# Kernel tuning notes

Measured on AMD Instinct MI355X. Metric: run time of the kernel, lower is better.

## Reference

```python
import jax, jax.numpy as jnp
import numpy as np

N, C, T, V = 64, 64, 300, 25  # batch, channels, frames, joints
CO = 64
EPS = 1e-5


def setup_inputs() -> dict:
    key = jax.random.key(0)
    ks = jax.random.split(key, 5)
    x = jax.random.normal(ks[0], (N, C, T, V), dtype=jnp.float32)
    lin_w = jax.random.normal(ks[1], (C, CO), dtype=jnp.float32) * np.sqrt(1.0 / CO)
    lin_b = jnp.zeros((1, 1, CO), dtype=jnp.float32)
    feat_mask = jax.random.normal(ks[2], (1, V, C), dtype=jnp.float32) * 0.1
    bn_gamma = jnp.ones((V * CO,), dtype=jnp.float32)
    bn_beta = jnp.zeros((V * CO,), dtype=jnp.float32)
    shift_in = jax.random.randint(ks[3], (V * C,), 0, V * C, dtype=jnp.int32)
    shift_out = jax.random.randint(ks[4], (V * CO,), 0, V * CO, dtype=jnp.int32)
    return {"x": x, "lin_w": lin_w, "lin_b": lin_b, "feat_mask": feat_mask,
            "bn_gamma": bn_gamma, "bn_beta": bn_beta,
            "shift_in": shift_in, "shift_out": shift_out}


def reference(x, lin_w, lin_b, feat_mask, bn_gamma, bn_beta, shift_in, shift_out):
    n, c, t, v = x.shape
    co = lin_w.shape[1]
    # (N,C,T,V) -> (N*T, V*C)
    xt = jnp.transpose(x, (0, 2, 3, 1)).reshape(n * t, v * c)
    # shift-in gather along feature axis
    xs = jnp.take(xt, shift_in, axis=1).reshape(n * t, v, c)
    # learned feature mask (tanh + 1)
    xs = xs * (jnp.tanh(feat_mask) + 1.0)
    # small channel-mixing matmul + bias
    y = jnp.einsum('nvc,cd->nvd', xs, lin_w) + lin_b  # (N*T, V, CO)
    y = y.reshape(n * t, v * co)
    # shift-out gather
    y = jnp.take(y, shift_out, axis=1)
    # BatchNorm1d (training mode: batch statistics over N*T)
    mean = jnp.mean(y, axis=0)
    var = jnp.mean(jnp.square(y - mean), axis=0)
    y = (y - mean) * jax.lax.rsqrt(var + EPS) * bn_gamma + bn_beta
    # back to (N, CO, T, V), residual (in==out -> identity down), ReLU
    y = jnp.transpose(y.reshape(n, t, v, co), (0, 3, 1, 2))
    return jax.nn.relu(y + x)
```

## Files before the change

### kernel.cpp

```cpp
#include <hip/hip_runtime.h>

typedef __bf16 bf16x8 __attribute__((ext_vector_type(8)));
typedef float f32x4 __attribute__((ext_vector_type(4)));
typedef unsigned short u16;
typedef unsigned int u32;
typedef unsigned long long u64;
typedef u16 u16x8 __attribute__((ext_vector_type(8)));

#define TID ((int)threadIdx.x)

constexpr int Nn = 64, Tt = 300, Vv = 25;
constexpr int Fin = 1600;
constexpr int RowsT = 19200;
constexpr int TBR = 16;
constexpr int NTB = 19;
constexpr int NBLK = Nn * NTB;
constexpr int RAWE = 64 * TBR * Vv;
constexpr float EPSv = 1e-5f;

constexpr int WS_EPI   = 12800;
constexpr int WS_WV    = 25600;
constexpr int WS_COMBO = 33792;
constexpr int WS_PART  = 40192;
constexpr size_t WS_NEED_PART = (size_t)WS_PART + (size_t)NBLK * 3200 * 4;

__device__ __forceinline__ u16 f2b(float f) {
  u32 u = __float_as_uint(f);
  return (u16)((u + 0x7fffu + ((u >> 16) & 1u)) >> 16);
}
__device__ __forceinline__ float b2f(u16 h) {
  return __uint_as_float(((u32)h) << 16);
}
__device__ __forceinline__ u64 pack4(float a, float b, float c, float d) {
  return (u64)f2b(a) | ((u64)f2b(b) << 16) | ((u64)f2b(c) << 32) | ((u64)f2b(d) << 48);
}

__device__ __forceinline__ void stage_raw(const float* __restrict__ x,
                                          int n, int t0, int validg, u16* raw) {
  const int base = n * 480000 + t0 * 25;
  if (validg == TBR * 25) {
    #pragma unroll
    for (int i = 0; i < 13; ++i) {
      int q = TID + i * 512;
      if (q < 6400) {
        int c = q / 100;
        int g4 = (q - c * 100) * 4;
        float4 xv = *reinterpret_cast<const float4*>(x + base + c * 7500 + g4);
        *reinterpret_cast<u64*>(raw + q * 4) = pack4(xv.x, xv.y, xv.z, xv.w);
      }
    }
  } else {
    #pragma unroll
    for (int i = 0; i < 13; ++i) {
      int q = TID + i * 512;
      if (q < 6400) {
        int c = q / 100;
        int g4 = (q - c * 100) * 4;
        float4 xv = make_float4(0.f, 0.f, 0.f, 0.f);
        if (g4 < validg)
          xv = *reinterpret_cast<const float4*>(x + base + c * 7500 + g4);
        *reinterpret_cast<u64*>(raw + q * 4) = pack4(xv.x, xv.y, xv.z, xv.w);
      }
    }
  }
}

__device__ __forceinline__ void load_bfr_g(const u16* __restrict__ wv, bf16x8 bfr[2][4]) {
  int l = TID & 63;
  #pragma unroll
  for (int ks = 0; ks < 2; ++ks)
    #pragma unroll
    for (int nt = 0; nt < 4; ++nt)
      bfr[ks][nt] = *reinterpret_cast<const bf16x8*>(wv + ((((ks << 2) | nt) << 9) + l * 8));
}

__device__ __forceinline__ bf16x8 build_a(const u16* raw, const u32* __restrict__ combo,
                                          int v, int ks, int t, int grp) {
  int jb = v * 64 + ks * 32 + grp * 8;
  bf16x8 a;
  #pragma unroll
  for (int i = 0; i < 8; ++i) {
    u32 cb = combo[jb + i];
    float m = __uint_as_float((cb & 0xffffu) << 16);
    float xv = b2f(raw[(cb >> 16) + t * 25]);
    a[i] = (__bf16)(xv * m);
  }
  return a;
}

__global__ void k_wv(const float* __restrict__ lin_w, const float* __restrict__ feat_mask,
                     const int* __restrict__ shift_in, float* __restrict__ wsum,
                     u16* __restrict__ wv, u32* __restrict__ combo_g) {
  int gid = blockIdx.x * 256 + TID;
  if (gid < 3200) wsum[gid] = 0.f;
  if (gid < Fin) {
    int s = shift_in[gid];
    u32 off = (u32)((s & 63) * 400 + (s >> 6));
    float m = tanhf(feat_mask[gid]) + 1.0f;
    combo_g[gid] = (off << 16) | (u32)f2b(m);
  }
  if (gid >= 2048 && gid < 2560) {
    int t = gid - 2048;
    int l = t & 63, nt = (t >> 6) & 3, ks = t >> 8;
    int c0 = ks * 32 + (l >> 4) * 8, d = nt * 16 + (l & 15);
    u16x8 o8;
    #pragma unroll
    for (int i = 0; i < 8; ++i) o8[i] = f2b(lin_w[(c0 + i) * 64 + d]);
    *reinterpret_cast<u16x8*>(wv + ((((ks << 2) | nt) << 9) + l * 8)) = o8;
  }
}

template <int ATOMIC>
__global__ __launch_bounds__(512, 6) void k_stats(
    const float* __restrict__ x, const u16* __restrict__ wv,
    const u32* __restrict__ combo_g, float* __restrict__ target)
{
  __shared__ __align__(16) u16 raw[RAWE];
  int bid = blockIdx.x;
  int n = bid / NTB, tb = bid - n * NTB;
  int t0 = tb * TBR;
  int validg = min(TBR, Tt - t0) * 25;
  int w = TID >> 6, l = TID & 63;
  int t_lane = l & 15, grp = l >> 4;

  stage_raw(x, n, t0, validg, raw);
  __syncthreads();

  bf16x8 areg[4][2];
  #pragma unroll
  for (int k = 0; k < 4; ++k) {
    int v = w + 8 * k;
    if (v < Vv) {
      areg[k][0] = build_a(raw, combo_g, v, 0, t_lane, grp);
      areg[k][1] = build_a(raw, combo_g, v, 1, t_lane, grp);
    }
  }

  bf16x8 bfr[2][4];
  load_bfr_g(wv, bfr);

  float* pb = target + (ATOMIC ? 0 : bid * 3200);
  #pragma unroll
  for (int k = 0; k < 4; ++k) {
    int v = w + 8 * k;
    if (v < Vv) {
      float pr[4], qr[4];
      #pragma unroll
      for (int nt = 0; nt < 4; ++nt) {
        f32x4 acc = {0.f, 0.f, 0.f, 0.f};
        acc = __builtin_amdgcn_mfma_f32_16x16x32_bf16(areg[k][0], bfr[0][nt], acc, 0, 0, 0);
        acc = __builtin_amdgcn_mfma_f32_16x16x32_bf16(areg[k][1], bfr[1][nt], acc, 0, 0, 0);
        float pp = acc[0] + acc[1] + acc[2] + acc[3];
        float qq = acc[0]*acc[0] + acc[1]*acc[1] + acc[2]*acc[2] + acc[3]*acc[3];
        pp += __shfl_xor(pp, 16); pp += __shfl_xor(pp, 32);
        qq += __shfl_xor(qq, 16); qq += __shfl_xor(qq, 32);
        pr[nt] = pp; qr[nt] = qq;
      }
      if (ATOMIC) {
        if ((l & 48) == 0) {
          #pragma unroll
          for (int nt = 0; nt < 4; ++nt) {
            int col = v * 64 + nt * 16 + t_lane;
            atomicAdd(&pb[col], pr[nt]);
            atomicAdd(&pb[1600 + col], qr[nt]);
          }
        }
      } else {
        float pv = (grp & 2) ? ((grp & 1) ? pr[3] : pr[2]) : ((grp & 1) ? pr[1] : pr[0]);
        float qv = (grp & 2) ? ((grp & 1) ? qr[3] : qr[2]) : ((grp & 1) ? qr[1] : qr[0]);
        pb[v * 64 + l] = pv;
        pb[1600 + v * 64 + l] = qv;
      }
    }
  }
}

__global__ __launch_bounds__(256) void k_red(const float* __restrict__ part,
                                             float* __restrict__ wsum) {
  __shared__ float red[16 * 17];
  int col0 = blockIdx.x * 16;
  int c = TID & 15, ch = TID >> 4;
  float s = 0.f;
  int r0 = ch * 76;
  #pragma unroll 4
  for (int i = 0; i < 76; ++i) s += part[(r0 + i) * 3200 + col0 + c];
  red[ch * 17 + c] = s;
  __syncthreads();
  if (TID < 16) {
    float t = 0.f;
    #pragma unroll
    for (int j = 0; j < 16; ++j) t += red[j * 17 + TID];
    wsum[col0 + TID] = t;
  }
}

__global__ void k_epi(const float* __restrict__ wsum, const float* __restrict__ gamma,
                      const float* __restrict__ beta, const int* __restrict__ shift_out,
                      u64* __restrict__ epi_g) {
  int k = blockIdx.x * 256 + TID;
  if (k >= Fin) return;
  int s2 = shift_out[k];
  float sm = wsum[s2] * (1.0f / RowsT);
  float sq = wsum[1600 + s2] * (1.0f / RowsT);
  float rstd = rsqrtf(fmaxf(sq - sm * sm, 0.f) + EPSv);
  float sc = gamma[k] * rstd;
  int d = k & 63, v = k >> 6;
  epi_g[d * 25 + v] = (u64)__float_as_uint(sc)
                    | ((u64)f2b(beta[k] - sm * sc) << 32)
                    | ((u64)(u32)(s2 * 16) << 48);
}

__global__ __launch_bounds__(512, 6) void k_main(
    const float* __restrict__ x, const u16* __restrict__ wv,
    const u32* __restrict__ combo_g, const u64* __restrict__ epi_g,
    float* __restrict__ out)
{
  __shared__ __align__(16) u16 smem[RAWE];
  u16* raw  = smem;
  u16* ylds = smem;

  int bid = blockIdx.x;
  int n = bid / NTB, tb = bid - n * NTB;
  int t0 = tb * TBR;
  int validg = min(TBR, Tt - t0) * 25;

  stage_raw(x, n, t0, validg, raw);
  __syncthreads();

  int w = TID >> 6, l = TID & 63, grp = l >> 4, t_lane = l & 15;
  bf16x8 areg[4][2];
  #pragma unroll
  for (int k = 0; k < 4; ++k) {
    int v = w + 8 * k;
    if (v < Vv) {
      areg[k][0] = build_a(raw, combo_g, v, 0, t_lane, grp);
      areg[k][1] = build_a(raw, combo_g, v, 1, t_lane, grp);
    }
  }
  __syncthreads();

  bf16x8 bfr[2][4];
  load_bfr_g(wv, bfr);

  #pragma unroll
  for (int k = 0; k < 4; ++k) {
    int v = w + 8 * k;
    if (v < Vv) {
      #pragma unroll
      for (int nt = 0; nt < 4; ++nt) {
        f32x4 acc = {0.f, 0.f, 0.f, 0.f};
        acc = __builtin_amdgcn_mfma_f32_16x16x32_bf16(areg[k][0], bfr[0][nt], acc, 0, 0, 0);
        acc = __builtin_amdgcn_mfma_f32_16x16x32_bf16(areg[k][1], bfr[1][nt], acc, 0, 0, 0);
        int col = v * 64 + nt * 16 + t_lane;
        int o = (col << 4) + ((grp ^ (col & 3)) << 2);
        *reinterpret_cast<u64*>(ylds + o) = pack4(acc[0], acc[1], acc[2], acc[3]);
      }
    }
  }
  __syncthreads();

  const int obase = n * 480000 + t0 * 25;
  #pragma unroll 2
  for (int it = 0; it < 13; ++it) {
    int g = TID + it * 512;
    if (g < 6400) {
      int d = g / 100;
      int f0 = (g - d * 100) * 4;
      if (f0 < validg) {
        const float4 xr = *reinterpret_cast<const float4*>(x + obase + d * 7500 + f0);
        float4 o;
        float* op = &o.x;
        const float* xp = &xr.x;
        #pragma unroll
        for (int e = 0; e < 4; ++e) {
          int f = f0 + e;
          int t = f / 25;
          int v = f - t * 25;
          u64 ep = epi_g[d * 25 + v];
          float sc = __uint_as_float((u32)ep);
          float of = b2f((u16)(ep >> 32));
          u32 bk = (u32)(ep >> 48);
          int elem = (int)bk + (t ^ (((bk >> 4) & 3) << 2));
          float y = b2f(ylds[elem]);
          op[e] = fmaxf(fmaf(y, sc, of) + xp[e], 0.f);
        }
        *reinterpret_cast<float4*>(out + obase + d * 7500 + f0) = o;
      }
    }
  }
}

extern "C" void kernel_launch(void* const* d_in, const int* in_sizes, int n_in,
                              void* d_out, int out_size, void* d_ws, size_t ws_size,
                              hipStream_t stream) {
  (void)in_sizes; (void)n_in; (void)out_size;
  const float* x        = (const float*)d_in[0];
  const float* lin_w    = (const float*)d_in[1];
  const float* feat_mask= (const float*)d_in[3];
  const float* gamma    = (const float*)d_in[4];
  const float* beta     = (const float*)d_in[5];
  const int*   shift_in = (const int*)d_in[6];
  const int*   shift_out= (const int*)d_in[7];
  float* wsum   = (float*)d_ws;
  u64*   epi_g  = (u64*)((char*)d_ws + WS_EPI);
  u16*   wv     = (u16*)((char*)d_ws + WS_WV);
  u32*   combo_g= (u32*)((char*)d_ws + WS_COMBO);
  float* part   = (float*)((char*)d_ws + WS_PART);

  k_wv<<<13, 256, 0, stream>>>(lin_w, feat_mask, shift_in, wsum, wv, combo_g);
  if (ws_size >= WS_NEED_PART) {
    k_stats<0><<<NBLK, 512, 0, stream>>>(x, wv, combo_g, part);
    k_red<<<200, 256, 0, stream>>>(part, wsum);
  } else {
    k_stats<1><<<NBLK, 512, 0, stream>>>(x, wv, combo_g, wsum);
  }
  k_epi <<<7, 256, 0, stream>>>(wsum, gamma, beta, shift_out, epi_g);
  k_main<<<NBLK, 512, 0, stream>>>(x, wv, combo_g, epi_g, (float*)d_out);
}
```

Measured before the change: 132.9 us.

## Retile time blocks to 12 frames, drop tail padding, stage epilogue table in LDS

Time tiles shrink from 16 frames to 12, so the 300 frames split evenly into 25 blocks. This removes the padded tail block and its bounds checks, and cuts the zero work done inside 16-row MFMA tiles. The y buffer in LDS moves to a row-major layout with padded stride 1604, and the epilogue scale/offset/index table is copied into LDS instead of being read from global memory per element. In exchange, a quarter of every MFMA tile is wasted on masked rows, and per-block LDS use and block count both rise.

```diff
diff --git a/kernel.cpp b/kernel.cpp
--- a/kernel.cpp
+++ b/kernel.cpp
@@ -12,10 +12,13 @@
 constexpr int Nn = 64, Tt = 300, Vv = 25;
 constexpr int Fin = 1600;
 constexpr int RowsT = 19200;
-constexpr int TBR = 16;
-constexpr int NTB = 19;
+constexpr int TBR = 12;
+constexpr int NTB = 25;
 constexpr int NBLK = Nn * NTB;
-constexpr int RAWE = 64 * TBR * Vv;
+constexpr int RAWE = 64 * 300;
+constexpr int YROW = 1604;
+constexpr int EPI_OFF = 38496;
+constexpr int SMEM_SZ = EPI_OFF + 12800;
 constexpr float EPSv = 1e-5f;
 
 constexpr int WS_EPI   = 12800;
@@ -36,31 +39,16 @@
 }
 
 __device__ __forceinline__ void stage_raw(const float* __restrict__ x,
-                                          int n, int t0, int validg, u16* raw) {
-  const int base = n * 480000 + t0 * 25;
-  if (validg == TBR * 25) {
-    #pragma unroll
-    for (int i = 0; i < 13; ++i) {
-      int q = TID + i * 512;
-      if (q < 6400) {
-        int c = q / 100;
-        int g4 = (q - c * 100) * 4;
-        float4 xv = *reinterpret_cast<const float4*>(x + base + c * 7500 + g4);
-        *reinterpret_cast<u64*>(raw + q * 4) = pack4(xv.x, xv.y, xv.z, xv.w);
-      }
-    }
-  } else {
-    #pragma unroll
-    for (int i = 0; i < 13; ++i) {
-      int q = TID + i * 512;
-      if (q < 6400) {
-        int c = q / 100;
-        int g4 = (q - c * 100) * 4;
-        float4 xv = make_float4(0.f, 0.f, 0.f, 0.f);
-        if (g4 < validg)
-          xv = *reinterpret_cast<const float4*>(x + base + c * 7500 + g4);
-        *reinterpret_cast<u64*>(raw + q * 4) = pack4(xv.x, xv.y, xv.z, xv.w);
-      }
+                                          int n, int tb, u16* raw) {
+  const int base = n * 480000 + tb * 300;
+  #pragma unroll
+  for (int i = 0; i < 10; ++i) {
+    int q = TID + i * 512;
+    if (q < 4800) {
+      int c = q / 75;
+      int g4 = (q - c * 75) * 4;
+      float4 xv = *reinterpret_cast<const float4*>(x + base + c * 7500 + g4);
+      *reinterpret_cast<u64*>(raw + q * 4) = pack4(xv.x, xv.y, xv.z, xv.w);
     }
   }
 }
@@ -84,6 +72,10 @@
     float m = __uint_as_float((cb & 0xffffu) << 16);
     float xv = b2f(raw[(cb >> 16) + t * 25]);
     a[i] = (__bf16)(xv * m);
+  }
+  if (t >= TBR) {
+    u64* p = reinterpret_cast<u64*>(&a);
+    p[0] = 0; p[1] = 0;
   }
   return a;
 }
@@ -95,7 +87,7 @@
   if (gid < 3200) wsum[gid] = 0.f;
   if (gid < Fin) {
     int s = shift_in[gid];
-    u32 off = (u32)((s & 63) * 400 + (s >> 6));
+    u32 off = (u32)((s & 63) * 300 + (s >> 6));
     float m = tanhf(feat_mask[gid]) + 1.0f;
     combo_g[gid] = (off << 16) | (u32)f2b(m);
   }
@@ -118,12 +110,10 @@
   __shared__ __align__(16) u16 raw[RAWE];
   int bid = blockIdx.x;
   int n = bid / NTB, tb = bid - n * NTB;
-  int t0 = tb * TBR;
-  int validg = min(TBR, Tt - t0) * 25;
   int w = TID >> 6, l = TID & 63;
   int t_lane = l & 15, grp = l >> 4;
 
-  stage_raw(x, n, t0, validg, raw);
+  stage_raw(x, n, tb, raw);
   __syncthreads();
 
   bf16x8 areg[4][2];
@@ -181,9 +171,9 @@
   int col0 = blockIdx.x * 16;
   int c = TID & 15, ch = TID >> 4;
   float s = 0.f;
-  int r0 = ch * 76;
+  int r0 = ch * 100;
   #pragma unroll 4
-  for (int i = 0; i < 76; ++i) s += part[(r0 + i) * 3200 + col0 + c];
+  for (int i = 0; i < 100; ++i) s += part[(r0 + i) * 3200 + col0 + c];
   red[ch * 17 + c] = s;
   __syncthreads();
   if (TID < 16) {
@@ -207,7 +197,7 @@
   int d = k & 63, v = k >> 6;
   epi_g[d * 25 + v] = (u64)__float_as_uint(sc)
                     | ((u64)f2b(beta[k] - sm * sc) << 32)
-                    | ((u64)(u32)(s2 * 16) << 48);
+                    | ((u64)(u32)s2 << 48);
 }
 
 __global__ __launch_bounds__(512, 6) void k_main(
@@ -215,16 +205,20 @@
     const u32* __restrict__ combo_g, const u64* __restrict__ epi_g,
     float* __restrict__ out)
 {
-  __shared__ __align__(16) u16 smem[RAWE];
-  u16* raw  = smem;
-  u16* ylds = smem;
+  __shared__ __align__(16) unsigned char smem[SMEM_SZ];
+  u16* raw  = reinterpret_cast<u16*>(smem);
+  u16* ylds = reinterpret_cast<u16*>(smem);
+  u64* epi  = reinterpret_cast<u64*>(smem + EPI_OFF);
 
   int bid = blockIdx.x;
   int n = bid / NTB, tb = bid - n * NTB;
-  int t0 = tb * TBR;
-  int validg = min(TBR, Tt - t0) * 25;
-
-  stage_raw(x, n, t0, validg, raw);
+
+  stage_raw(x, n, tb, raw);
+  #pragma unroll
+  for (int i = 0; i < 4; ++i) {
+    int j = TID + i * 512;
+    if (j < Fin) epi[j] = epi_g[j];
+  }
   __syncthreads();
 
   int w = TID >> 6, l = TID & 63, grp = l >> 4, t_lane = l & 15;
@@ -251,41 +245,40 @@
         f32x4 acc = {0.f, 0.f, 0.f, 0.f};
         acc = __builtin_amdgcn_mfma_f32_16x16x32_bf16(areg[k][0], bfr[0][nt], acc, 0, 0, 0);
         acc = __builtin_amdgcn_mfma_f32_16x16x32_bf16(areg[k][1], bfr[1][nt], acc, 0, 0, 0);
-        int col = v * 64 + nt * 16 + t_lane;
-        int o = (col << 4) + ((grp ^ (col & 3)) << 2);
-        *reinterpret_cast<u64*>(ylds + o) = pack4(acc[0], acc[1], acc[2], acc[3]);
+        if (grp < 3) {
+          int col = v * 64 + nt * 16 + t_lane;
+          #pragma unroll
+          for (int j = 0; j < 4; ++j)
+            ylds[(grp * 4 + j) * YROW + col] = f2b(acc[j]);
+        }
       }
     }
   }
   __syncthreads();
 
-  const int obase = n * 480000 + t0 * 25;
-  #pragma unroll 2
-  for (int it = 0; it < 13; ++it) {
+  const int obase = n * 480000 + tb * 300;
+  #pragma unroll
+  for (int it = 0; it < 10; ++it) {
     int g = TID + it * 512;
-    if (g < 6400) {
-      int d = g / 100;
-      int f0 = (g - d * 100) * 4;
-      if (f0 < validg) {
-        const float4 xr = *reinterpret_cast<const float4*>(x + obase + d * 7500 + f0);
-        float4 o;
-        float* op = &o.x;
-        const float* xp = &xr.x;
-        #pragma unroll
-        for (int e = 0; e < 4; ++e) {
-          int f = f0 + e;
-          int t = f / 25;
-          int v = f - t * 25;
-          u64 ep = epi_g[d * 25 + v];
-          float sc = __uint_as_float((u32)ep);
-          float of = b2f((u16)(ep >> 32));
-          u32 bk = (u32)(ep >> 48);
-          int elem = (int)bk + (t ^ (((bk >> 4) & 3) << 2));
-          float y = b2f(ylds[elem]);
-          op[e] = fmaxf(fmaf(y, sc, of) + xp[e], 0.f);
-        }
-        *reinterpret_cast<float4*>(out + obase + d * 7500 + f0) = o;
+    if (g < 4800) {
+      int d = g / 75;
+      int f0 = (g - d * 75) * 4;
+      const float4 xr = *reinterpret_cast<const float4*>(x + obase + d * 7500 + f0);
+      float4 o;
+      float* op = &o.x;
+      const float* xp = &xr.x;
+      #pragma unroll
+      for (int e = 0; e < 4; ++e) {
+        int f = f0 + e;
+        int t = f / 25;
+        int v = f - t * 25;
+        u64 ep = epi[d * 25 + v];
+        float sc = __uint_as_float((u32)ep);
+        float of = b2f((u16)(ep >> 32));
+        float y = b2f(ylds[t * YROW + (int)(ep >> 48)]);
+        op[e] = fmaxf(fmaf(y, sc, of) + xp[e], 0.f);
       }
+      *reinterpret_cast<float4*>(out + obase + d * 7500 + f0) = o;
     }
   }
 }
```

New measurement: 237.8 us. 1.79x slower.
